# Performance work log

Hardware: AMD Instinct MI355X
Metric: run time of the kernel (lower is better)

The kernel has to match this reference:

```python
import jax, jax.numpy as jnp
import numpy as np

EPS2 = 0.01 ** 2   # Plummer softening squared (cfg.v_phi_eps ** 2)
C_STRENGTH = 1.0   # cfg.v_phi_C


def _gelu(x):
    # torch F.gelu default = exact (erf) form
    return jax.nn.gelu(x, approximate=False)


def _pair_dist2(a, b):
    # ||a_t - b_s||^2 via squared-norm expansion; (B,T,d),(B,S,d) -> (B,T,S)
    a2 = jnp.sum(a * a, axis=-1)[:, :, None]
    b2 = jnp.sum(b * b, axis=-1)[:, None, :]
    ab = jnp.einsum('btd,bsd->bts', a, b)
    return jnp.maximum(a2 + b2 - 2.0 * ab, 0.0)


def setup_inputs() -> dict:
    key = jax.random.key(0)
    B, T, d = 8, 512, 128
    dl, K, Hp, Ht = 16, 8, 32, 32
    s = 0.02  # v_phi_init_scale
    ks = jax.random.split(key, 12)
    return {
        'h':        jax.random.normal(ks[0], (B, T, d), dtype=jnp.float32),
        'h_src':    jax.random.normal(ks[1], (B, T, d), dtype=jnp.float32),
        # W_l : Linear(d, dl, bias=False)
        'W_l':      s * jax.random.normal(ks[2], (dl, d), dtype=jnp.float32),
        # W_theta : Linear(d, K, bias=False)
        'W_theta':  s * jax.random.normal(ks[3], (K, d), dtype=jnp.float32),
        # phi_c_net : Linear(1,Hp) -> GELU -> Linear(Hp,1)
        'phi_w1':   s * jax.random.normal(ks[4], (Hp, 1), dtype=jnp.float32),
        'phi_b1':   jnp.zeros((Hp,), dtype=jnp.float32),
        'phi_w2':   s * jax.random.normal(ks[5], (1, Hp), dtype=jnp.float32),
        'phi_b2':   jnp.zeros((1,), dtype=jnp.float32),
        # theta aligner
        'tw_q':     s * jax.random.normal(ks[6], (Ht, K), dtype=jnp.float32),
        'tw_s':     s * jax.random.normal(ks[7], (Ht, K), dtype=jnp.float32),
        'tw_d':     s * jax.random.normal(ks[8], (Ht, K), dtype=jnp.float32),
        'theta_b1': jnp.zeros((Ht,), dtype=jnp.float32),
        'tw2_w':    s * jax.random.normal(ks[9], (1, Ht), dtype=jnp.float32),
        'tw2_b':    jnp.zeros((1,), dtype=jnp.float32),
    }


def reference(h, h_src, W_l, W_theta, phi_w1, phi_b1, phi_w2, phi_b2,
              tw_q, tw_s, tw_d, theta_b1, tw2_w, tw2_b):
    # type / angle projections
    l_q = jnp.einsum('btd,ld->btl', h, W_l)
    l_s = jnp.einsum('btd,ld->btl', h_src, W_l)
    th_q = jnp.einsum('btd,kd->btk', h, W_theta)
    th_s = jnp.einsum('btd,kd->btk', h_src, W_theta)

    # Gaussian gate Phi with learned per-pair inverse bandwidth c
    l_dist2 = _pair_dist2(l_q, l_s)                       # (B,T,T)
    hid = _gelu(l_dist2[..., None] * phi_w1[:, 0] + phi_b1)  # (B,T,T,Hp)
    c = jax.nn.softplus(hid @ phi_w2[0] + phi_b2[0])      # (B,T,T)
    Phi = jnp.exp(-c * l_dist2)

    # bounded value-aligner Theta (low-rank bilinear MLP over pairs)
    proj_t = th_q @ tw_q.T + th_q @ tw_d.T + theta_b1     # (B,T,Ht)
    proj_u = th_s @ tw_s.T - th_s @ tw_d.T                # (B,T,Ht)
    hidden = _gelu(proj_t[:, :, None, :] + proj_u[:, None, :, :])  # (B,T,T,Ht)
    Theta = jnp.tanh(hidden @ tw2_w[0] + tw2_b[0])        # (B,T,T)

    # Plummer-softened 1/r factor
    r = jnp.sqrt(_pair_dist2(h, h_src) + EPS2)
    return -C_STRENGTH * Theta * Phi / r
```

## Files before the change

kernel.cpp:

```cpp
#include <hip/hip_runtime.h>
#include <hip/hip_bf16.h>
#include <math.h>

#define T 512
#define EPS2 1e-4f
#define C0G 0.79788456f
#define C1G (-0.13298076f)
#define C2G (0.019947114f)
#define C3G (-0.0023746564f)

typedef __attribute__((ext_vector_type(8))) short s8v;
typedef __attribute__((ext_vector_type(4))) float f4v;

__device__ __forceinline__ uint pk2(float a, float b){
  __hip_bfloat162 t = __float22bfloat162_rn(make_float2(a, b));
  return *reinterpret_cast<uint*>(&t);
}
__device__ __forceinline__ ushort f2bf(float x){
  __hip_bfloat16 t = __float2bfloat16(x);
  return *reinterpret_cast<ushort*>(&t);
}
__device__ __forceinline__ float bflo(uint u){ return __uint_as_float(u<<16); }
__device__ __forceinline__ float bfhi(uint u){ return __uint_as_float(u & 0xFFFF0000u); }
#define MFMA32 __builtin_amdgcn_mfma_f32_16x16x32_bf16
__device__ __forceinline__ float gf(float x){ float x2=x*x; return x + x2*fmaf(C1G,x2,C0G); }

#define L_HA   0
#define L_HB0  16384
#define L_HB1  32768
#define L_WB   49152
#define L_UVT  70912
#define L_UVS0 84224
#define L_UVS1 97536
#define L_LPT  110848
#define L_LPS0 113920
#define L_LPS1 116992
#define L_K    120064
#define L_TOT  120128

__global__ __launch_bounds__(512,1) void k_all(
    const float* __restrict__ h, const float* __restrict__ hsrc,
    const float* __restrict__ Wl, const float* __restrict__ Wt,
    const float* __restrict__ pw1, const float* __restrict__ pb1,
    const float* __restrict__ pw2, const float* __restrict__ pb2,
    const float* __restrict__ twq, const float* __restrict__ tws,
    const float* __restrict__ twd, const float* __restrict__ tb1,
    const float* __restrict__ tw2, const float* __restrict__ tb2,
    float* __restrict__ out)
{
  extern __shared__ __align__(16) char smem[];
  ushort* hA   = (ushort*)(smem + L_HA);
  ushort* hB0  = (ushort*)(smem + L_HB0);
  ushort* hB1  = (ushort*)(smem + L_HB1);
  ushort* Wb   = (ushort*)(smem + L_WB);
  ushort* uvT  = (ushort*)(smem + L_UVT);
  ushort* uvS0 = (ushort*)(smem + L_UVS0);
  ushort* uvS1 = (ushort*)(smem + L_UVS1);

  const int tid = threadIdx.x;
  const int Lb  = blockIdx.x;
  const int blk = ((Lb & 7) << 5) | (Lb >> 3);
  const int b   = blk >> 5;
  const int bt  = ((blk >> 2) & 7) * 64;
  const int bs0 = (blk & 3) * 128;
  const int lane = tid & 63, wv = tid >> 6;
  const int hi = lane >> 4, c = lane & 15;
  const int sside = wv >> 2, strip = wv & 3, q0 = sside*2;

  #pragma unroll
  for (int it=0; it<6; ++it){
    const int i = tid + it*512;
    const int tile = i >> 10, i1 = i & 1023;
    const int row = i1 >> 4, cid = i1 & 15;
    const int kk = cid >> 2, h2 = cid & 3;
    const float* base = (tile==0) ? h + (unsigned)(b*T + bt)*128u
                                  : hsrc + (unsigned)(b*T + bs0 + (tile==2?64:0))*128u;
    const float4* src = (const float4*)(base + (unsigned)row*128u + kk*32 + h2*8);
    const float4 a0 = src[0], a1 = src[1];
    uint4 v; v.x=pk2(a0.x,a0.y); v.y=pk2(a0.z,a0.w); v.z=pk2(a1.x,a1.y); v.w=pk2(a1.z,a1.w);
    ushort* dst = (tile==0) ? hA : (tile==1 ? hB0 : hB1);
    *(uint4*)(dst + ((row>>4)*256 + kk*64 + h2*16 + (row&15))*8) = v;
  }
  if (tid < 256){
    const int j = tid>>4, k0 = (tid&15)*8;
    const float4* src = (const float4*)(Wl + j*128 + k0);
    const float4 b0 = src[0], b1 = src[1];
    uint4 v; v.x=pk2(b0.x,b0.y); v.y=pk2(b0.z,b0.w); v.z=pk2(b1.x,b1.y); v.w=pk2(b1.z,b1.w);
    *(uint4*)(Wb + j*136 + k0) = v;
  }
  {
    const int sideF = tid>>8, j=(tid>>3)&31, k0=(tid&7)*16;
    float tw[8];
    #pragma unroll
    for (int m=0;m<8;m++){
      const float d = twd[j*8+m];
      tw[m] = sideF ? (tws[j*8+m]-d) : (twq[j*8+m]+d);
    }
    float o[16];
    #pragma unroll
    for (int i=0;i<16;i++) o[i]=0.f;
    #pragma unroll
    for (int m=0;m<8;m++){
      const float4* wr = (const float4*)(Wt + m*128 + k0);
      #pragma unroll
      for (int g=0; g<4; ++g){
        const float4 qv = wr[g];
        o[g*4+0]=fmaf(tw[m],qv.x,o[g*4+0]); o[g*4+1]=fmaf(tw[m],qv.y,o[g*4+1]);
        o[g*4+2]=fmaf(tw[m],qv.z,o[g*4+2]); o[g*4+3]=fmaf(tw[m],qv.w,o[g*4+3]);
      }
    }
    ushort* dst = Wb + (16 + sideF*32 + j)*136 + k0;
    uint4 v;
    v.x=pk2(o[0],o[1]); v.y=pk2(o[2],o[3]); v.z=pk2(o[4],o[5]); v.w=pk2(o[6],o[7]);
    *(uint4*)dst = v;
    v.x=pk2(o[8],o[9]); v.y=pk2(o[10],o[11]); v.z=pk2(o[12],o[13]); v.w=pk2(o[14],o[15]);
    *(uint4*)(dst+8) = v;
  }
  __syncthreads();

  const float w2a = tw2[c], w2b = tw2[c+16];
  const float tb2v = tb2[0];

  #define PROJ_PACK(SRC_TILE, WROW0, IS_T, UVDST, LPOFF)                        \
  {                                                                             \
    f4v p0={0,0,0,0}, p1={0,0,0,0}, p2={0,0,0,0};                               \
    float nrm = 0.f;                                                            \
    _Pragma("unroll")                                                           \
    for (int kk=0;kk<4;kk++){                                                   \
      union { s8v s; uint4 u; } U;                                              \
      U.s = *(const s8v*)((SRC_TILE) + (strip*256 + kk*64 + lane)*8);           \
      { float x;                                                                \
        x=bflo(U.u.x); nrm=fmaf(x,x,nrm); x=bfhi(U.u.x); nrm=fmaf(x,x,nrm);     \
        x=bflo(U.u.y); nrm=fmaf(x,x,nrm); x=bfhi(U.u.y); nrm=fmaf(x,x,nrm);     \
        x=bflo(U.u.z); nrm=fmaf(x,x,nrm); x=bfhi(U.u.z); nrm=fmaf(x,x,nrm);     \
        x=bflo(U.u.w); nrm=fmaf(x,x,nrm); x=bfhi(U.u.w); nrm=fmaf(x,x,nrm); }   \
      const int ko = kk*32 + hi*8;                                              \
      const s8v bl = *(const s8v*)(Wb + (c)*136 + ko);                          \
      const s8v b0 = *(const s8v*)(Wb + ((WROW0) + c)*136 + ko);                \
      const s8v b1 = *(const s8v*)(Wb + ((WROW0) + 16 + c)*136 + ko);           \
      p0 = MFMA32(U.s, b0, p0,0,0,0);                                           \
      p1 = MFMA32(U.s, b1, p1,0,0,0);                                           \
      p2 = MFMA32(U.s, bl, p2,0,0,0);                                           \
    }                                                                           \
    nrm += __shfl_xor(nrm,16); nrm += __shfl_xor(nrm,32);                       \
    char* lpBase = smem + (LPOFF);                                              \
    if (hi==0) *(float*)(lpBase + (strip*16 + c)*48 + 32) = nrm;                \
    _Pragma("unroll")                                                           \
    for (int r=0;r<4;r++){                                                      \
      const int row = strip*16 + hi*4 + r;                                      \
      const float a0 = p0[r] + ((IS_T) ? tb1[c]    : 0.f);                      \
      const float a1 = p1[r] + ((IS_T) ? tb1[c+16] : 0.f);                      \
      const float lv = p2[r];                                                   \
      float pab = fmaf(w2a, gf(a0), w2b*gf(a1));                                \
      float pl  = lv*lv;                                                        \
      _Pragma("unroll")                                                         \
      for (int m=1;m<16;m<<=1){ pab += __shfl_xor(pab,m); pl += __shfl_xor(pl,m); } \
      if (c==0){                                                                \
        float* hb_ = (float*)(lpBase + row*48 + 32);                            \
        hb_[1] = pl;                                                            \
        hb_[2] = (IS_T) ? fmaf(0.5f, pab, tb2v) : 0.5f*pab;                     \
      }                                                                         \
      ((ushort*)(lpBase))[row*24 + c] = f2bf(lv);                               \
      const float a02=a0*a0, a12=a1*a1;                                         \
      if (IS_T){                                                                \
        const float wa0 = w2a*a0, wa1 = w2b*a1;                                 \
        *(uint*)((UVDST) + row*104 +      2*c) = pk2(wa0*fmaf(2.f*C1G, a02, C0G), \
                                                     wa1*fmaf(2.f*C1G, a12, C0G)); \
        *(uint*)((UVDST) + row*104 + 32 + 2*c) = pk2(3.f*C1G*w2a*a02, 3.f*C1G*w2b*a12); \
        *(uint*)((UVDST) + row*104 + 64 + 2*c) = pk2(2.f*C1G*wa0, 2.f*C1G*wa1); \
      } else {                                                                  \
        *(uint*)((UVDST) + row*104 +      2*c) = pk2(a0, a1);                   \
        *(uint*)((UVDST) + row*104 + 32 + 2*c) = pk2(a02, a12);                 \
        *(uint*)((UVDST) + row*104 + 64 + 2*c) = pk2(a02*a0, a12*a1);           \
      }                                                                         \
    }                                                                           \
  }

  if (sside == 0){
    PROJ_PACK(hA, 16, 1, uvT, L_LPT)
  } else {
    PROJ_PACK(hB0, 48, 0, uvS0, L_LPS0)
  }
  if (sside == 0){
    PROJ_PACK(hB1, 48, 0, uvS1, L_LPS1)
  } else if (wv == 4){
    const int lj = lane & 31;
    const float kw = (lane < 32) ? (0.5f * pw2[lj]) : 0.f;
    const float bb = pb1[lj], mm = pw1[lj];
    float bp[9], mp[9];
    bp[0]=1.f; mp[0]=1.f;
    #pragma unroll
    for (int i=1;i<9;i++){ bp[i]=bp[i-1]*bb; mp[i]=mp[i-1]*mm; }
    float Kq[9];
    Kq[0] = kw*(bb + C0G*bp[2] + C1G*bp[4] + C2G*bp[6] + C3G*bp[8]);
    Kq[1] = kw*mp[1]*(1.f + 2.f*C0G*bp[1] + 4.f*C1G*bp[3] + 6.f*C2G*bp[5] + 8.f*C3G*bp[7]);
    Kq[2] = kw*mp[2]*(C0G + 6.f*C1G*bp[2] + 15.f*C2G*bp[4] + 28.f*C3G*bp[6]);
    Kq[3] = kw*mp[3]*(4.f*C1G*bp[1] + 20.f*C2G*bp[3] + 56.f*C3G*bp[5]);
    Kq[4] = kw*mp[4]*(C1G + 15.f*C2G*bp[2] + 70.f*C3G*bp[4]);
    Kq[5] = kw*mp[5]*(6.f*C2G*bp[1] + 56.f*C3G*bp[3]);
    Kq[6] = kw*mp[6]*(C2G + 28.f*C3G*bp[2]);
    Kq[7] = kw*mp[7]*(8.f*C3G*bp[1]);
    Kq[8] = kw*mp[8]*C3G;
    #pragma unroll
    for (int m=1;m<64;m<<=1){
      #pragma unroll
      for (int i=0;i<9;i++) Kq[i] += __shfl_xor(Kq[i], m);
    }
    if (lane==0){
      Kq[0] += pb2[0];
      #pragma unroll
      for (int i=0;i<9;i++) ((float*)(smem+L_K))[i] = Kq[i];
    }
  }
  #undef PROJ_PACK
  __syncthreads();

  float K[9];
  #pragma unroll
  for (int i=0;i<9;i++) K[i] = ((const float*)(smem+L_K))[i];
  s8v ah[4];
  #pragma unroll
  for (int kk=0;kk<4;kk++) ah[kk] = *(const s8v*)(hA + (strip*256 + kk*64 + lane)*8);

  #define PAIR_PHASE(HBX, UVSX, LPSOFF, BS)                                     \
  {                                                                             \
    f4v acch[2], accz[2], accl[2];                                              \
    _Pragma("unroll")                                                           \
    for (int qq=0;qq<2;qq++){ acch[qq]=(f4v){0,0,0,0}; accz[qq]=(f4v){0,0,0,0}; accl[qq]=(f4v){0,0,0,0}; } \
    _Pragma("unroll")                                                           \
    for (int kk=0;kk<4;kk++){                                                   \
      _Pragma("unroll")                                                         \
      for (int qq=0;qq<2;qq++)                                                  \
        acch[qq] = MFMA32(ah[kk], *(const s8v*)((HBX) + ((q0+qq)*256 + kk*64 + lane)*8), acch[qq],0,0,0); \
    }                                                                           \
    _Pragma("unroll")                                                           \
    for (int ks=0;ks<3;ks++){                                                   \
      const s8v au = *(const s8v*)(uvT + (strip*16 + c)*104 + ks*32 + hi*8);    \
      _Pragma("unroll")                                                         \
      for (int qq=0;qq<2;qq++)                                                  \
        accz[qq] = MFMA32(au, *(const s8v*)((UVSX) + ((q0+qq)*16 + c)*104 + ks*32 + hi*8), accz[qq],0,0,0); \
    }                                                                           \
    {                                                                           \
      union { uint4 u; s8v s; } Z; Z.u = make_uint4(0,0,0,0);                   \
      const s8v al_ = (hi<2) ? *(const s8v*)(smem + L_LPT + (strip*16+c)*48 + hi*16) : Z.s; \
      _Pragma("unroll")                                                         \
      for (int qq=0;qq<2;qq++){                                                 \
        const s8v bq = (hi<2) ? *(const s8v*)(smem + (LPSOFF) + ((q0+qq)*16+c)*48 + hi*16) : Z.s; \
        accl[qq] = MFMA32(al_, bq, accl[qq],0,0,0);                             \
      }                                                                         \
    }                                                                           \
    float h2t[4], l2t[4], alv[4];                                               \
    _Pragma("unroll")                                                           \
    for (int r=0;r<4;r++){                                                      \
      const float* th_ = (const float*)(smem + L_LPT + (strip*16 + hi*4 + r)*48 + 32); \
      h2t[r]=th_[0]; l2t[r]=th_[1]; alv[r]=th_[2];                              \
    }                                                                           \
    _Pragma("unroll")                                                           \
    for (int qq=0;qq<2;qq++){                                                   \
      const int sidx = (q0+qq)*16 + c;                                          \
      const float* sh_ = (const float*)(smem + (LPSOFF) + sidx*48 + 32);        \
      const float h2s=sh_[0], l2s=sh_[1], bet=sh_[2];                           \
      _Pragma("unroll")                                                         \
      for (int r=0;r<4;r++){                                                    \
        const float d2 = fmaxf(fmaf(-2.f, acch[qq][r], h2t[r] + h2s), 0.f);     \
        const float ir = rsqrtf(d2 + EPS2);                                     \
        const float l2 = fmaxf(fmaf(-2.f, accl[qq][r], l2t[r] + l2s), 0.f);     \
        const float lam = fminf(l2, 16.f);                                      \
        float zc = K[8];                                                        \
        _Pragma("unroll")                                                       \
        for (int i=7;i>=0;i--) zc = fmaf(zc, lam, K[i]);                        \
        const float cc  = __logf(1.f + __expf(zc));                             \
        const float phi = __expf(-cc * l2);                                     \
        const float z   = accz[qq][r] + alv[r] + bet;                           \
        const float th  = z * fmaf(z*z, -0.33333334f, 1.f);                     \
        __builtin_nontemporal_store(-th * phi * ir,                             \
          out + (unsigned)(b*T + bt + strip*16 + hi*4 + r)*T + (BS) + sidx);    \
      }                                                                         \
    }                                                                           \
  }

  PAIR_PHASE(hB0, uvS0, L_LPS0, bs0)
  PAIR_PHASE(hB1, uvS1, L_LPS1, bs0 + 64)
  #undef PAIR_PHASE
}

extern "C" void kernel_launch(void* const* d_in, const int* in_sizes, int n_in,
                              void* d_out, int out_size, void* d_ws, size_t ws_size,
                              hipStream_t stream) {
  const float* h    = (const float*)d_in[0];
  const float* hsrc = (const float*)d_in[1];
  const float* Wl   = (const float*)d_in[2];
  const float* Wt   = (const float*)d_in[3];
  const float* pw1  = (const float*)d_in[4];
  const float* pb1  = (const float*)d_in[5];
  const float* pw2  = (const float*)d_in[6];
  const float* pb2  = (const float*)d_in[7];
  const float* twq  = (const float*)d_in[8];
  const float* tws  = (const float*)d_in[9];
  const float* twd  = (const float*)d_in[10];
  const float* tb1  = (const float*)d_in[11];
  const float* tw2  = (const float*)d_in[12];
  const float* tb2  = (const float*)d_in[13];
  float* out = (float*)d_out;

  hipFuncSetAttribute((const void*)k_all,
                      hipFuncAttributeMaxDynamicSharedMemorySize, L_TOT);
  k_all<<<dim3(256,1,1), dim3(512,1,1), L_TOT, stream>>>(
      h,hsrc,Wl,Wt,pw1,pb1,pw2,pb2,twq,tws,twd,tb1,tw2,tb2,out);
}
```

Baseline: 18.94 us.

## Shrink shared memory by aliasing buffers to raise block occupancy

Reorganises the shared-memory layout so the weight and uv/lp buffers alias the hA staging area, and uses a single source-side uv/lp buffer that is repacked between the two pair phases. Projections are now computed into registers first, then packed after a barrier, and the second source half is packed only after the first pair phase finishes. Launch bounds change from 1 to 4 blocks per multiprocessor, aiming at more resident waves to hide latency. The cost is extra barriers, more live registers holding projection results, and serialisation of the second pack step.

```diff
diff --git a/kernel.cpp b/kernel.cpp
--- a/kernel.cpp
+++ b/kernel.cpp
@@ -26,19 +26,17 @@
 __device__ __forceinline__ float gf(float x){ float x2=x*x; return x + x2*fmaf(C1G,x2,C0G); }
 
 #define L_HA   0
-#define L_HB0  16384
-#define L_HB1  32768
-#define L_WB   49152
-#define L_UVT  70912
-#define L_UVS0 84224
-#define L_UVS1 97536
-#define L_LPT  110848
-#define L_LPS0 113920
-#define L_LPS1 116992
-#define L_K    120064
-#define L_TOT  120128
-
-__global__ __launch_bounds__(512,1) void k_all(
+#define L_WB   16384
+#define L_UVT  0
+#define L_UVS  13312
+#define L_LPT  26624
+#define L_LPS  29696
+#define L_HB0  38144
+#define L_HB1  54528
+#define L_K    70912
+#define L_TOT  70976
+
+__global__ __launch_bounds__(512,4) void k_all(
     const float* __restrict__ h, const float* __restrict__ hsrc,
     const float* __restrict__ Wl, const float* __restrict__ Wt,
     const float* __restrict__ pw1, const float* __restrict__ pb1,
@@ -49,13 +47,12 @@
     float* __restrict__ out)
 {
   extern __shared__ __align__(16) char smem[];
-  ushort* hA   = (ushort*)(smem + L_HA);
-  ushort* hB0  = (ushort*)(smem + L_HB0);
-  ushort* hB1  = (ushort*)(smem + L_HB1);
-  ushort* Wb   = (ushort*)(smem + L_WB);
-  ushort* uvT  = (ushort*)(smem + L_UVT);
-  ushort* uvS0 = (ushort*)(smem + L_UVS0);
-  ushort* uvS1 = (ushort*)(smem + L_UVS1);
+  ushort* hA  = (ushort*)(smem + L_HA);
+  ushort* hB0 = (ushort*)(smem + L_HB0);
+  ushort* hB1 = (ushort*)(smem + L_HB1);
+  ushort* Wb  = (ushort*)(smem + L_WB);
+  ushort* uvT = (ushort*)(smem + L_UVT);
+  ushort* uvS = (ushort*)(smem + L_UVS);
 
   const int tid = threadIdx.x;
   const int Lb  = blockIdx.x;
@@ -118,170 +115,187 @@
   }
   __syncthreads();
 
+  #define PROJ_REG(SRC_TILE, WROW0, P0, P1, P2v, NRM)                          \
+  {                                                                            \
+    _Pragma("unroll")                                                          \
+    for (int kk=0;kk<4;kk++){                                                  \
+      union { s8v s; uint4 u; } U;                                             \
+      U.s = *(const s8v*)((SRC_TILE) + (strip*256 + kk*64 + lane)*8);          \
+      { float x;                                                               \
+        x=bflo(U.u.x); NRM=fmaf(x,x,NRM); x=bfhi(U.u.x); NRM=fmaf(x,x,NRM);    \
+        x=bflo(U.u.y); NRM=fmaf(x,x,NRM); x=bfhi(U.u.y); NRM=fmaf(x,x,NRM);    \
+        x=bflo(U.u.z); NRM=fmaf(x,x,NRM); x=bfhi(U.u.z); NRM=fmaf(x,x,NRM);    \
+        x=bflo(U.u.w); NRM=fmaf(x,x,NRM); x=bfhi(U.u.w); NRM=fmaf(x,x,NRM); }  \
+      const int ko = kk*32 + hi*8;                                             \
+      const s8v bl = *(const s8v*)(Wb + (c)*136 + ko);                         \
+      const s8v b0 = *(const s8v*)(Wb + ((WROW0) + c)*136 + ko);               \
+      const s8v b1 = *(const s8v*)(Wb + ((WROW0) + 16 + c)*136 + ko);          \
+      P0 = MFMA32(U.s, b0, P0,0,0,0);                                          \
+      P1 = MFMA32(U.s, b1, P1,0,0,0);                                          \
+      P2v = MFMA32(U.s, bl, P2v,0,0,0);                                        \
+    }                                                                          \
+    NRM += __shfl_xor(NRM,16); NRM += __shfl_xor(NRM,32);                      \
+  }
+
+  s8v ah[4];
+  #pragma unroll
+  for (int kk=0;kk<4;kk++) ah[kk] = *(const s8v*)(hA + (strip*256 + kk*64 + lane)*8);
+
+  f4v tp0={0,0,0,0}, tp1={0,0,0,0}, tp2={0,0,0,0};  float tn = 0.f;
+  f4v sp0={0,0,0,0}, sp1={0,0,0,0}, sp2={0,0,0,0};  float sn = 0.f;
+  if (sside == 0){
+    PROJ_REG(hA, 16, tp0, tp1, tp2, tn)
+    PROJ_REG(hB1, 48, sp0, sp1, sp2, sn)
+  } else {
+    PROJ_REG(hB0, 48, tp0, tp1, tp2, tn)
+  }
+  #undef PROJ_REG
+  __syncthreads();
+
   const float w2a = tw2[c], w2b = tw2[c+16];
   const float tb2v = tb2[0];
 
-  #define PROJ_PACK(SRC_TILE, WROW0, IS_T, UVDST, LPOFF)                        \
-  {                                                                             \
-    f4v p0={0,0,0,0}, p1={0,0,0,0}, p2={0,0,0,0};                               \
-    float nrm = 0.f;                                                            \
-    _Pragma("unroll")                                                           \
-    for (int kk=0;kk<4;kk++){                                                   \
-      union { s8v s; uint4 u; } U;                                              \
-      U.s = *(const s8v*)((SRC_TILE) + (strip*256 + kk*64 + lane)*8);           \
-      { float x;                                                                \
-        x=bflo(U.u.x); nrm=fmaf(x,x,nrm); x=bfhi(U.u.x); nrm=fmaf(x,x,nrm);     \
-        x=bflo(U.u.y); nrm=fmaf(x,x,nrm); x=bfhi(U.u.y); nrm=fmaf(x,x,nrm);     \
-        x=bflo(U.u.z); nrm=fmaf(x,x,nrm); x=bfhi(U.u.z); nrm=fmaf(x,x,nrm);     \
-        x=bflo(U.u.w); nrm=fmaf(x,x,nrm); x=bfhi(U.u.w); nrm=fmaf(x,x,nrm); }   \
-      const int ko = kk*32 + hi*8;                                              \
-      const s8v bl = *(const s8v*)(Wb + (c)*136 + ko);                          \
-      const s8v b0 = *(const s8v*)(Wb + ((WROW0) + c)*136 + ko);                \
-      const s8v b1 = *(const s8v*)(Wb + ((WROW0) + 16 + c)*136 + ko);           \
-      p0 = MFMA32(U.s, b0, p0,0,0,0);                                           \
-      p1 = MFMA32(U.s, b1, p1,0,0,0);                                           \
-      p2 = MFMA32(U.s, bl, p2,0,0,0);                                           \
-    }                                                                           \
-    nrm += __shfl_xor(nrm,16); nrm += __shfl_xor(nrm,32);                       \
-    char* lpBase = smem + (LPOFF);                                              \
-    if (hi==0) *(float*)(lpBase + (strip*16 + c)*48 + 32) = nrm;                \
-    _Pragma("unroll")                                                           \
-    for (int r=0;r<4;r++){                                                      \
-      const int row = strip*16 + hi*4 + r;                                      \
-      const float a0 = p0[r] + ((IS_T) ? tb1[c]    : 0.f);                      \
-      const float a1 = p1[r] + ((IS_T) ? tb1[c+16] : 0.f);                      \
-      const float lv = p2[r];                                                   \
-      float pab = fmaf(w2a, gf(a0), w2b*gf(a1));                                \
-      float pl  = lv*lv;                                                        \
-      _Pragma("unroll")                                                         \
+  #define PACK(P0, P1, P2v, NRM, IS_T, UVDST, LPOFF)                           \
+  {                                                                            \
+    char* lpBase = smem + (LPOFF);                                             \
+    if (hi==0) *(float*)(lpBase + (strip*16 + c)*48 + 32) = NRM;               \
+    _Pragma("unroll")                                                          \
+    for (int r=0;r<4;r++){                                                     \
+      const int row = strip*16 + hi*4 + r;                                     \
+      const float a0 = P0[r] + ((IS_T) ? tb1[c]    : 0.f);                     \
+      const float a1 = P1[r] + ((IS_T) ? tb1[c+16] : 0.f);                     \
+      const float lv = P2v[r];                                                 \
+      float pab = fmaf(w2a, gf(a0), w2b*gf(a1));                               \
+      float pl  = lv*lv;                                                       \
+      _Pragma("unroll")                                                        \
       for (int m=1;m<16;m<<=1){ pab += __shfl_xor(pab,m); pl += __shfl_xor(pl,m); } \
-      if (c==0){                                                                \
-        float* hb_ = (float*)(lpBase + row*48 + 32);                            \
-        hb_[1] = pl;                                                            \
-        hb_[2] = (IS_T) ? fmaf(0.5f, pab, tb2v) : 0.5f*pab;                     \
-      }                                                                         \
-      ((ushort*)(lpBase))[row*24 + c] = f2bf(lv);                               \
-      const float a02=a0*a0, a12=a1*a1;                                         \
-      if (IS_T){                                                                \
-        const float wa0 = w2a*a0, wa1 = w2b*a1;                                 \
+      if (c==0){                                                               \
+        float* hb_ = (float*)(lpBase + row*48 + 32);                           \
+        hb_[1] = pl;                                                           \
+        hb_[2] = (IS_T) ? fmaf(0.5f, pab, tb2v) : 0.5f*pab;                    \
+      }                                                                        \
+      ((ushort*)(lpBase))[row*24 + c] = f2bf(lv);                              \
+      const float a02=a0*a0, a12=a1*a1;                                        \
+      if (IS_T){                                                               \
+        const float wa0 = w2a*a0, wa1 = w2b*a1;                                \
         *(uint*)((UVDST) + row*104 +      2*c) = pk2(wa0*fmaf(2.f*C1G, a02, C0G), \
                                                      wa1*fmaf(2.f*C1G, a12, C0G)); \
         *(uint*)((UVDST) + row*104 + 32 + 2*c) = pk2(3.f*C1G*w2a*a02, 3.f*C1G*w2b*a12); \
-        *(uint*)((UVDST) + row*104 + 64 + 2*c) = pk2(2.f*C1G*wa0, 2.f*C1G*wa1); \
-      } else {                                                                  \
-        *(uint*)((UVDST) + row*104 +      2*c) = pk2(a0, a1);                   \
-        *(uint*)((UVDST) + row*104 + 32 + 2*c) = pk2(a02, a12);                 \
-        *(uint*)((UVDST) + row*104 + 64 + 2*c) = pk2(a02*a0, a12*a1);           \
-      }                                                                         \
-    }                                                                           \
+        *(uint*)((UVDST) + row*104 + 64 + 2*c) = pk2(2.f*C1G*wa0, 2.f*C1G*wa1);\
+      } else {                                                                 \
+        *(uint*)((UVDST) + row*104 +      2*c) = pk2(a0, a1);                  \
+        *(uint*)((UVDST) + row*104 + 32 + 2*c) = pk2(a02, a12);                \
+        *(uint*)((UVDST) + row*104 + 64 + 2*c) = pk2(a02*a0, a12*a1);          \
+      }                                                                        \
+    }                                                                          \
   }
 
   if (sside == 0){
-    PROJ_PACK(hA, 16, 1, uvT, L_LPT)
+    PACK(tp0, tp1, tp2, tn, 1, uvT, L_LPT)
   } else {
-    PROJ_PACK(hB0, 48, 0, uvS0, L_LPS0)
-  }
-  if (sside == 0){
-    PROJ_PACK(hB1, 48, 0, uvS1, L_LPS1)
-  } else if (wv == 4){
-    const int lj = lane & 31;
-    const float kw = (lane < 32) ? (0.5f * pw2[lj]) : 0.f;
-    const float bb = pb1[lj], mm = pw1[lj];
-    float bp[9], mp[9];
-    bp[0]=1.f; mp[0]=1.f;
-    #pragma unroll
-    for (int i=1;i<9;i++){ bp[i]=bp[i-1]*bb; mp[i]=mp[i-1]*mm; }
-    float Kq[9];
-    Kq[0] = kw*(bb + C0G*bp[2] + C1G*bp[4] + C2G*bp[6] + C3G*bp[8]);
-    Kq[1] = kw*mp[1]*(1.f + 2.f*C0G*bp[1] + 4.f*C1G*bp[3] + 6.f*C2G*bp[5] + 8.f*C3G*bp[7]);
-    Kq[2] = kw*mp[2]*(C0G + 6.f*C1G*bp[2] + 15.f*C2G*bp[4] + 28.f*C3G*bp[6]);
-    Kq[3] = kw*mp[3]*(4.f*C1G*bp[1] + 20.f*C2G*bp[3] + 56.f*C3G*bp[5]);
-    Kq[4] = kw*mp[4]*(C1G + 15.f*C2G*bp[2] + 70.f*C3G*bp[4]);
-    Kq[5] = kw*mp[5]*(6.f*C2G*bp[1] + 56.f*C3G*bp[3]);
-    Kq[6] = kw*mp[6]*(C2G + 28.f*C3G*bp[2]);
-    Kq[7] = kw*mp[7]*(8.f*C3G*bp[1]);
-    Kq[8] = kw*mp[8]*C3G;
-    #pragma unroll
-    for (int m=1;m<64;m<<=1){
+    PACK(tp0, tp1, tp2, tn, 0, uvS, L_LPS)
+    if (wv == 4){
+      const int lj = lane & 31;
+      const float kw = (lane < 32) ? (0.5f * pw2[lj]) : 0.f;
+      const float bb = pb1[lj], mm = pw1[lj];
+      float bp[9], mp[9];
+      bp[0]=1.f; mp[0]=1.f;
       #pragma unroll
-      for (int i=0;i<9;i++) Kq[i] += __shfl_xor(Kq[i], m);
+      for (int i=1;i<9;i++){ bp[i]=bp[i-1]*bb; mp[i]=mp[i-1]*mm; }
+      float Kq[9];
+      Kq[0] = kw*(bb + C0G*bp[2] + C1G*bp[4] + C2G*bp[6] + C3G*bp[8]);
+      Kq[1] = kw*mp[1]*(1.f + 2.f*C0G*bp[1] + 4.f*C1G*bp[3] + 6.f*C2G*bp[5] + 8.f*C3G*bp[7]);
+      Kq[2] = kw*mp[2]*(C0G + 6.f*C1G*bp[2] + 15.f*C2G*bp[4] + 28.f*C3G*bp[6]);
+      Kq[3] = kw*mp[3]*(4.f*C1G*bp[1] + 20.f*C2G*bp[3] + 56.f*C3G*bp[5]);
+      Kq[4] = kw*mp[4]*(C1G + 15.f*C2G*bp[2] + 70.f*C3G*bp[4]);
+      Kq[5] = kw*mp[5]*(6.f*C2G*bp[1] + 56.f*C3G*bp[3]);
+      Kq[6] = kw*mp[6]*(C2G + 28.f*C3G*bp[2]);
+      Kq[7] = kw*mp[7]*(8.f*C3G*bp[1]);
+      Kq[8] = kw*mp[8]*C3G;
+      #pragma unroll
+      for (int m=1;m<64;m<<=1){
+        #pragma unroll
+        for (int i=0;i<9;i++) Kq[i] += __shfl_xor(Kq[i], m);
+      }
+      if (lane==0){
+        Kq[0] += pb2[0];
+        #pragma unroll
+        for (int i=0;i<9;i++) ((float*)(smem+L_K))[i] = Kq[i];
+      }
     }
-    if (lane==0){
-      Kq[0] += pb2[0];
-      #pragma unroll
-      for (int i=0;i<9;i++) ((float*)(smem+L_K))[i] = Kq[i];
-    }
-  }
-  #undef PROJ_PACK
+  }
   __syncthreads();
 
   float K[9];
   #pragma unroll
   for (int i=0;i<9;i++) K[i] = ((const float*)(smem+L_K))[i];
-  s8v ah[4];
-  #pragma unroll
-  for (int kk=0;kk<4;kk++) ah[kk] = *(const s8v*)(hA + (strip*256 + kk*64 + lane)*8);
-
-  #define PAIR_PHASE(HBX, UVSX, LPSOFF, BS)                                     \
-  {                                                                             \
-    f4v acch[2], accz[2], accl[2];                                              \
-    _Pragma("unroll")                                                           \
+
+  #define PAIR_PHASE(HBX, BS)                                                  \
+  {                                                                            \
+    f4v acch[2], accz[2], accl[2];                                             \
+    _Pragma("unroll")                                                          \
     for (int qq=0;qq<2;qq++){ acch[qq]=(f4v){0,0,0,0}; accz[qq]=(f4v){0,0,0,0}; accl[qq]=(f4v){0,0,0,0}; } \
-    _Pragma("unroll")                                                           \
-    for (int kk=0;kk<4;kk++){                                                   \
-      _Pragma("unroll")                                                         \
-      for (int qq=0;qq<2;qq++)                                                  \
+    _Pragma("unroll")                                                          \
+    for (int kk=0;kk<4;kk++){                                                  \
+      _Pragma("unroll")                                                        \
+      for (int qq=0;qq<2;qq++)                                                 \
         acch[qq] = MFMA32(ah[kk], *(const s8v*)((HBX) + ((q0+qq)*256 + kk*64 + lane)*8), acch[qq],0,0,0); \
-    }                                                                           \
-    _Pragma("unroll")                                                           \
-    for (int ks=0;ks<3;ks++){                                                   \
-      const s8v au = *(const s8v*)(uvT + (strip*16 + c)*104 + ks*32 + hi*8);    \
-      _Pragma("unroll")                                                         \
-      for (int qq=0;qq<2;qq++)                                                  \
-        accz[qq] = MFMA32(au, *(const s8v*)((UVSX) + ((q0+qq)*16 + c)*104 + ks*32 + hi*8), accz[qq],0,0,0); \
-    }                                                                           \
-    {                                                                           \
-      union { uint4 u; s8v s; } Z; Z.u = make_uint4(0,0,0,0);                   \
+    }                                                                          \
+    _Pragma("unroll")                                                          \
+    for (int ks=0;ks<3;ks++){                                                  \
+      const s8v au = *(const s8v*)(uvT + (strip*16 + c)*104 + ks*32 + hi*8);   \
+      _Pragma("unroll")                                                        \
+      for (int qq=0;qq<2;qq++)                                                 \
+        accz[qq] = MFMA32(au, *(const s8v*)(uvS + ((q0+qq)*16 + c)*104 + ks*32 + hi*8), accz[qq],0,0,0); \
+    }                                                                          \
+    {                                                                          \
+      union { uint4 u; s8v s; } Z; Z.u = make_uint4(0,0,0,0);                  \
       const s8v al_ = (hi<2) ? *(const s8v*)(smem + L_LPT + (strip*16+c)*48 + hi*16) : Z.s; \
-      _Pragma("unroll")                                                         \
-      for (int qq=0;qq<2;qq++){                                                 \
-        const s8v bq = (hi<2) ? *(const s8v*)(smem + (LPSOFF) + ((q0+qq)*16+c)*48 + hi*16) : Z.s; \
-        accl[qq] = MFMA32(al_, bq, accl[qq],0,0,0);                             \
-      }                                                                         \
-    }                                                                           \
-    float h2t[4], l2t[4], alv[4];                                               \
-    _Pragma("unroll")                                                           \
-    for (int r=0;r<4;r++){                                                      \
+      _Pragma("unroll")                                                        \
+      for (int qq=0;qq<2;qq++){                                                \
+        const s8v bq = (hi<2) ? *(const s8v*)(smem + L_LPS + ((q0+qq)*16+c)*48 + hi*16) : Z.s; \
+        accl[qq] = MFMA32(al_, bq, accl[qq],0,0,0);                            \
+      }                                                                        \
+    }                                                                          \
+    float h2t[4], l2t[4], alv[4];                                              \
+    _Pragma("unroll")                                                          \
+    for (int r=0;r<4;r++){                                                     \
       const float* th_ = (const float*)(smem + L_LPT + (strip*16 + hi*4 + r)*48 + 32); \
-      h2t[r]=th_[0]; l2t[r]=th_[1]; alv[r]=th_[2];                              \
-    }                                                                           \
-    _Pragma("unroll")                                                           \
-    for (int qq=0;qq<2;qq++){                                                   \
-      const int sidx = (q0+qq)*16 + c;                                          \
-      const float* sh_ = (const float*)(smem + (LPSOFF) + sidx*48 + 32);        \
-      const float h2s=sh_[0], l2s=sh_[1], bet=sh_[2];                           \
-      _Pragma("unroll")                                                         \
-      for (int r=0;r<4;r++){                                                    \
-        const float d2 = fmaxf(fmaf(-2.f, acch[qq][r], h2t[r] + h2s), 0.f);     \
-        const float ir = rsqrtf(d2 + EPS2);                                     \
-        const float l2 = fmaxf(fmaf(-2.f, accl[qq][r], l2t[r] + l2s), 0.f);     \
-        const float lam = fminf(l2, 16.f);                                      \
-        float zc = K[8];                                                        \
-        _Pragma("unroll")                                                       \
-        for (int i=7;i>=0;i--) zc = fmaf(zc, lam, K[i]);                        \
-        const float cc  = __logf(1.f + __expf(zc));                             \
-        const float phi = __expf(-cc * l2);                                     \
-        const float z   = accz[qq][r] + alv[r] + bet;                           \
-        const float th  = z * fmaf(z*z, -0.33333334f, 1.f);                     \
-        __builtin_nontemporal_store(-th * phi * ir,                             \
-          out + (unsigned)(b*T + bt + strip*16 + hi*4 + r)*T + (BS) + sidx);    \
-      }                                                                         \
-    }                                                                           \
-  }
-
-  PAIR_PHASE(hB0, uvS0, L_LPS0, bs0)
-  PAIR_PHASE(hB1, uvS1, L_LPS1, bs0 + 64)
+      h2t[r]=th_[0]; l2t[r]=th_[1]; alv[r]=th_[2];                             \
+    }                                                                          \
+    _Pragma("unroll")                                                          \
+    for (int qq=0;qq<2;qq++){                                                  \
+      const int sidx = (q0+qq)*16 + c;                                         \
+      const float* sh_ = (const float*)(smem + L_LPS + sidx*48 + 32);          \
+      const float h2s=sh_[0], l2s=sh_[1], bet=sh_[2];                          \
+      _Pragma("unroll")                                                        \
+      for (int r=0;r<4;r++){                                                   \
+        const float d2 = fmaxf(fmaf(-2.f, acch[qq][r], h2t[r] + h2s), 0.f);    \
+        const float ir = rsqrtf(d2 + EPS2);                                    \
+        const float l2 = fmaxf(fmaf(-2.f, accl[qq][r], l2t[r] + l2s), 0.f);    \
+        const float lam = fminf(l2, 16.f);                                     \
+        float zc = K[8];                                                       \
+        _Pragma("unroll")                                                      \
+        for (int i=7;i>=0;i--) zc = fmaf(zc, lam, K[i]);                       \
+        const float cc  = __logf(1.f + __expf(zc));                            \
+        const float phi = __expf(-cc * l2);                                    \
+        const float z   = accz[qq][r] + alv[r] + bet;                          \
+        const float th  = z * fmaf(z*z, -0.33333334f, 1.f);                    \
+        __builtin_nontemporal_store(-th * phi * ir,                            \
+          out + (unsigned)(b*T + bt + strip*16 + hi*4 + r)*T + (BS) + sidx);   \
+      }                                                                        \
+    }                                                                          \
+  }
+
+  PAIR_PHASE(hB0, bs0)
+  __syncthreads();
+  if (sside == 0){
+    PACK(sp0, sp1, sp2, sn, 0, uvS, L_LPS)
+  }
+  __syncthreads();
+  PAIR_PHASE(hB1, bs0 + 64)
   #undef PAIR_PHASE
+  #undef PACK
 }
 
 extern "C" void kernel_launch(void* const* d_in, const int* in_sizes, int n_in,
```

Measured after the change: 20.39 us. +7.6%, slower.

## Double block size to 1024 threads and split pair phases across wave groups

Applied to the files above, without the earlier changes.

Raises the block from 512 to 1024 threads (16 waves) so each wave handles one of the two source half-tiles instead of looping over both pair phases serially. The projection/packing work is spread over three wave groups plus one wave for the gate-polynomial coefficients, instead of two groups doing two rounds. The aim is more waves in flight per CU to hide latency and shorten each wave's serial chain. In exchange, registers per thread are capped lower by the 1024-thread launch bound, which may cause spills.

```diff
diff --git a/kernel.cpp b/kernel.cpp
--- a/kernel.cpp
+++ b/kernel.cpp
@@ -38,7 +38,7 @@
 #define L_K    120064
 #define L_TOT  120128
 
-__global__ __launch_bounds__(512,1) void k_all(
+__global__ __launch_bounds__(1024,1) void k_all(
     const float* __restrict__ h, const float* __restrict__ hsrc,
     const float* __restrict__ Wl, const float* __restrict__ Wt,
     const float* __restrict__ pw1, const float* __restrict__ pb1,
@@ -65,11 +65,11 @@
   const int bs0 = (blk & 3) * 128;
   const int lane = tid & 63, wv = tid >> 6;
   const int hi = lane >> 4, c = lane & 15;
-  const int sside = wv >> 2, strip = wv & 3, q0 = sside*2;
-
-  #pragma unroll
-  for (int it=0; it<6; ++it){
-    const int i = tid + it*512;
+  const int strip = wv & 3, grp = wv >> 2;
+
+  #pragma unroll
+  for (int it=0; it<3; ++it){
+    const int i = tid + it*1024;
     const int tile = i >> 10, i1 = i & 1023;
     const int row = i1 >> 4, cid = i1 & 15;
     const int kk = cid >> 2, h2 = cid & 3;
@@ -88,7 +88,7 @@
     uint4 v; v.x=pk2(b0.x,b0.y); v.y=pk2(b0.z,b0.w); v.z=pk2(b1.x,b1.y); v.w=pk2(b1.z,b1.w);
     *(uint4*)(Wb + j*136 + k0) = v;
   }
-  {
+  if (tid < 512){
     const int sideF = tid>>8, j=(tid>>3)&31, k0=(tid&7)*16;
     float tw[8];
     #pragma unroll
@@ -176,14 +176,13 @@
     }                                                                           \
   }
 
-  if (sside == 0){
+  if (grp == 0){
     PROJ_PACK(hA, 16, 1, uvT, L_LPT)
-  } else {
+  } else if (grp == 1){
     PROJ_PACK(hB0, 48, 0, uvS0, L_LPS0)
-  }
-  if (sside == 0){
+  } else if (grp == 2){
     PROJ_PACK(hB1, 48, 0, uvS1, L_LPS1)
-  } else if (wv == 4){
+  } else if (wv == 12){
     const int lj = lane & 31;
     const float kw = (lane < 32) ? (0.5f * pw2[lj]) : 0.f;
     const float bb = pb1[lj], mm = pw1[lj];
@@ -222,66 +221,66 @@
   #pragma unroll
   for (int kk=0;kk<4;kk++) ah[kk] = *(const s8v*)(hA + (strip*256 + kk*64 + lane)*8);
 
-  #define PAIR_PHASE(HBX, UVSX, LPSOFF, BS)                                     \
-  {                                                                             \
-    f4v acch[2], accz[2], accl[2];                                              \
-    _Pragma("unroll")                                                           \
-    for (int qq=0;qq<2;qq++){ acch[qq]=(f4v){0,0,0,0}; accz[qq]=(f4v){0,0,0,0}; accl[qq]=(f4v){0,0,0,0}; } \
-    _Pragma("unroll")                                                           \
-    for (int kk=0;kk<4;kk++){                                                   \
-      _Pragma("unroll")                                                         \
-      for (int qq=0;qq<2;qq++)                                                  \
-        acch[qq] = MFMA32(ah[kk], *(const s8v*)((HBX) + ((q0+qq)*256 + kk*64 + lane)*8), acch[qq],0,0,0); \
-    }                                                                           \
-    _Pragma("unroll")                                                           \
-    for (int ks=0;ks<3;ks++){                                                   \
-      const s8v au = *(const s8v*)(uvT + (strip*16 + c)*104 + ks*32 + hi*8);    \
-      _Pragma("unroll")                                                         \
-      for (int qq=0;qq<2;qq++)                                                  \
-        accz[qq] = MFMA32(au, *(const s8v*)((UVSX) + ((q0+qq)*16 + c)*104 + ks*32 + hi*8), accz[qq],0,0,0); \
-    }                                                                           \
-    {                                                                           \
-      union { uint4 u; s8v s; } Z; Z.u = make_uint4(0,0,0,0);                   \
-      const s8v al_ = (hi<2) ? *(const s8v*)(smem + L_LPT + (strip*16+c)*48 + hi*16) : Z.s; \
-      _Pragma("unroll")                                                         \
-      for (int qq=0;qq<2;qq++){                                                 \
-        const s8v bq = (hi<2) ? *(const s8v*)(smem + (LPSOFF) + ((q0+qq)*16+c)*48 + hi*16) : Z.s; \
-        accl[qq] = MFMA32(al_, bq, accl[qq],0,0,0);                             \
-      }                                                                         \
-    }                                                                           \
-    float h2t[4], l2t[4], alv[4];                                               \
-    _Pragma("unroll")                                                           \
-    for (int r=0;r<4;r++){                                                      \
-      const float* th_ = (const float*)(smem + L_LPT + (strip*16 + hi*4 + r)*48 + 32); \
-      h2t[r]=th_[0]; l2t[r]=th_[1]; alv[r]=th_[2];                              \
-    }                                                                           \
-    _Pragma("unroll")                                                           \
-    for (int qq=0;qq<2;qq++){                                                   \
-      const int sidx = (q0+qq)*16 + c;                                          \
-      const float* sh_ = (const float*)(smem + (LPSOFF) + sidx*48 + 32);        \
-      const float h2s=sh_[0], l2s=sh_[1], bet=sh_[2];                           \
-      _Pragma("unroll")                                                         \
-      for (int r=0;r<4;r++){                                                    \
-        const float d2 = fmaxf(fmaf(-2.f, acch[qq][r], h2t[r] + h2s), 0.f);     \
-        const float ir = rsqrtf(d2 + EPS2);                                     \
-        const float l2 = fmaxf(fmaf(-2.f, accl[qq][r], l2t[r] + l2s), 0.f);     \
-        const float lam = fminf(l2, 16.f);                                      \
-        float zc = K[8];                                                        \
-        _Pragma("unroll")                                                       \
-        for (int i=7;i>=0;i--) zc = fmaf(zc, lam, K[i]);                        \
-        const float cc  = __logf(1.f + __expf(zc));                             \
-        const float phi = __expf(-cc * l2);                                     \
-        const float z   = accz[qq][r] + alv[r] + bet;                           \
-        const float th  = z * fmaf(z*z, -0.33333334f, 1.f);                     \
-        __builtin_nontemporal_store(-th * phi * ir,                             \
-          out + (unsigned)(b*T + bt + strip*16 + hi*4 + r)*T + (BS) + sidx);    \
-      }                                                                         \
-    }                                                                           \
-  }
-
-  PAIR_PHASE(hB0, uvS0, L_LPS0, bs0)
-  PAIR_PHASE(hB1, uvS1, L_LPS1, bs0 + 64)
-  #undef PAIR_PHASE
+  const int qh = wv >> 2;
+  const ushort* HBX  = (qh < 2) ? hB0 : hB1;
+  const ushort* UVSX = (qh < 2) ? uvS0 : uvS1;
+  const int LPSOFF   = (qh < 2) ? L_LPS0 : L_LPS1;
+  const int q0 = (qh & 1) * 2;
+  const int BS = bs0 + ((qh >= 2) ? 64 : 0);
+
+  f4v acch[2], accz[2], accl[2];
+  #pragma unroll
+  for (int qq=0;qq<2;qq++){ acch[qq]=(f4v){0,0,0,0}; accz[qq]=(f4v){0,0,0,0}; accl[qq]=(f4v){0,0,0,0}; }
+  #pragma unroll
+  for (int kk=0;kk<4;kk++){
+    #pragma unroll
+    for (int qq=0;qq<2;qq++)
+      acch[qq] = MFMA32(ah[kk], *(const s8v*)(HBX + ((q0+qq)*256 + kk*64 + lane)*8), acch[qq],0,0,0);
+  }
+  #pragma unroll
+  for (int ks=0;ks<3;ks++){
+    const s8v au = *(const s8v*)(uvT + (strip*16 + c)*104 + ks*32 + hi*8);
+    #pragma unroll
+    for (int qq=0;qq<2;qq++)
+      accz[qq] = MFMA32(au, *(const s8v*)(UVSX + ((q0+qq)*16 + c)*104 + ks*32 + hi*8), accz[qq],0,0,0);
+  }
+  {
+    union { uint4 u; s8v s; } Z; Z.u = make_uint4(0,0,0,0);
+    const s8v al_ = (hi<2) ? *(const s8v*)(smem + L_LPT + (strip*16+c)*48 + hi*16) : Z.s;
+    #pragma unroll
+    for (int qq=0;qq<2;qq++){
+      const s8v bq = (hi<2) ? *(const s8v*)(smem + LPSOFF + ((q0+qq)*16+c)*48 + hi*16) : Z.s;
+      accl[qq] = MFMA32(al_, bq, accl[qq],0,0,0);
+    }
+  }
+  float h2t[4], l2t[4], alv[4];
+  #pragma unroll
+  for (int r=0;r<4;r++){
+    const float* th_ = (const float*)(smem + L_LPT + (strip*16 + hi*4 + r)*48 + 32);
+    h2t[r]=th_[0]; l2t[r]=th_[1]; alv[r]=th_[2];
+  }
+  #pragma unroll
+  for (int qq=0;qq<2;qq++){
+    const int sidx = (q0+qq)*16 + c;
+    const float* sh_ = (const float*)(smem + LPSOFF + sidx*48 + 32);
+    const float h2s=sh_[0], l2s=sh_[1], bet=sh_[2];
+    #pragma unroll
+    for (int r=0;r<4;r++){
+      const float d2 = fmaxf(fmaf(-2.f, acch[qq][r], h2t[r] + h2s), 0.f);
+      const float ir = rsqrtf(d2 + EPS2);
+      const float l2 = fmaxf(fmaf(-2.f, accl[qq][r], l2t[r] + l2s), 0.f);
+      const float lam = fminf(l2, 16.f);
+      float zc = K[8];
+      #pragma unroll
+      for (int i=7;i>=0;i--) zc = fmaf(zc, lam, K[i]);
+      const float cc  = __logf(1.f + __expf(zc));
+      const float phi = __expf(-cc * l2);
+      const float z   = accz[qq][r] + alv[r] + bet;
+      const float th  = z * fmaf(z*z, -0.33333334f, 1.f);
+      __builtin_nontemporal_store(-th * phi * ir,
+        out + (unsigned)(b*T + bt + strip*16 + hi*4 + r)*T + BS + sidx);
+    }
+  }
 }
 
 extern "C" void kernel_launch(void* const* d_in, const int* in_sizes, int n_in,
@@ -305,6 +304,6 @@
 
   hipFuncSetAttribute((const void*)k_all,
                       hipFuncAttributeMaxDynamicSharedMemorySize, L_TOT);
-  k_all<<<dim3(256,1,1), dim3(512,1,1), L_TOT, stream>>>(
+  k_all<<<dim3(256,1,1), dim3(1024,1,1), L_TOT, stream>>>(
       h,hsrc,Wl,Wt,pw1,pb1,pw2,pb2,twq,tws,twd,tb1,tw2,tb2,out);
 }
```

Result: faster. 18.28 us (-3.5%).
